# Optimization experiments

Hardware: AMD Instinct MI355X
Metric: run time of the kernel (lower is better)

The kernel has to match this reference:

```python
import jax, jax.numpy as jnp
import numpy as np

N_LEVELS = 16
N_FEATS = 2
LOG2_T = 19
BASE_RES = 16.0
FINEST_RES = 512.0
N_POINTS = 1048576

_PRIMES = jnp.array([1, 2654435761, 805459861], dtype=jnp.uint32)
_OFFSETS = jnp.array([[i, j, k] for i in (0, 1) for j in (0, 1) for k in (0, 1)], dtype=jnp.int32)  # [8,3]
_MASK = jnp.uint32(2 ** LOG2_T - 1)


def setup_inputs() -> dict:
    key = jax.random.key(0)
    k1, k2 = jax.random.split(key)
    x = jax.random.uniform(k1, (N_POINTS, 3), dtype=jnp.float32)
    # nn.init.uniform_(w, a=-1e-4, b=1e-4) per level; stacked [L, T, F]
    embeddings = jax.random.uniform(k2, (N_LEVELS, 2 ** LOG2_T, N_FEATS),
                                    dtype=jnp.float32, minval=-1e-4, maxval=1e-4)
    bounding_box = jnp.stack([jnp.zeros(3, jnp.float32), jnp.ones(3, jnp.float32)])  # [2,3]
    return {"x": x, "embeddings": embeddings, "bounding_box": bounding_box}


def _resolutions():
    b = np.exp((np.log(FINEST_RES) - np.log(BASE_RES)) / (N_LEVELS - 1))
    return jnp.asarray(np.floor(BASE_RES * b ** np.arange(N_LEVELS)), dtype=jnp.float32)  # [L]


def reference(x, embeddings, bounding_box):
    box_min, box_max = bounding_box[0], bounding_box[1]
    keep_mask = jnp.all((x >= box_min) & (x <= box_max), axis=-1)  # [N]
    xc = jnp.clip(x, box_min, box_max)  # clamped coords used for voxel indexing

    def level(emb, res):
        grid = (box_max - box_min) / res                              # [3]
        bl = jnp.floor((xc - box_min) / grid).astype(jnp.int32)       # [N,3] bottom-left voxel idx
        vmin = bl.astype(x.dtype) * grid + box_min                    # [N,3]
        w = (x - vmin) / grid                                         # [N,3] (original x, as in source)
        corners = bl[:, None, :] + _OFFSETS[None]                     # [N,8,3]
        h = corners.astype(jnp.uint32) * _PRIMES                      # wrap-around uint32 mul
        hashed = ((h[..., 0] ^ h[..., 1] ^ h[..., 2]) & _MASK).astype(jnp.int32)  # [N,8]
        v = emb[hashed]                                               # [N,8,F] gather
        wx, wy, wz = w[:, 0:1], w[:, 1:2], w[:, 2:3]
        c00 = v[:, 0] * (1 - wx) + v[:, 4] * wx
        c01 = v[:, 1] * (1 - wx) + v[:, 5] * wx
        c10 = v[:, 2] * (1 - wx) + v[:, 6] * wx
        c11 = v[:, 3] * (1 - wx) + v[:, 7] * wx
        c0 = c00 * (1 - wy) + c10 * wy
        c1 = c01 * (1 - wy) + c11 * wy
        return c0 * (1 - wz) + c1 * wz                                # [N,F]

    feats = jax.vmap(level)(embeddings, _resolutions())               # [L,N,F]
    out = jnp.transpose(feats, (1, 0, 2)).reshape(x.shape[0], N_LEVELS * N_FEATS)  # level-major concat
    return out, keep_mask
```

## Files before the change

kernel.cpp:

```cpp
#include <hip/hip_runtime.h>
#include <math.h>
#include <stdint.h>


#define NLEVELS 16
#define NFINE 10
#define HASH_MASK 0x7FFFFu
#define TABLE_ENTRIES 524288

typedef float f32x2 __attribute__((ext_vector_type(2)));
typedef float f32x4 __attribute__((ext_vector_type(4)));

struct ResTable { float r[NLEVELS]; };
struct PairMeta { int dim[6]; int off[6]; };

__device__ __forceinline__ float2 gather_one_level(
    const float* __restrict__ x, const float2* __restrict__ tbl,
    float bmin0, float bmin1, float bmin2,
    float bmax0, float bmax1, float bmax2,
    float res, int point)
{
    const float* xp = x + (size_t)point * 3;
    float x0 = __builtin_nontemporal_load(xp + 0);
    float x1 = __builtin_nontemporal_load(xp + 1);
    float x2 = __builtin_nontemporal_load(xp + 2);

    float xc0 = fminf(fmaxf(x0, bmin0), bmax0);
    float xc1 = fminf(fmaxf(x1, bmin1), bmax1);
    float xc2 = fminf(fmaxf(x2, bmin2), bmax2);

    float g0 = (bmax0 - bmin0) / res;
    float g1 = (bmax1 - bmin1) / res;
    float g2 = (bmax2 - bmin2) / res;

    float f0 = floorf((xc0 - bmin0) / g0);
    float f1 = floorf((xc1 - bmin1) / g1);
    float f2 = floorf((xc2 - bmin2) / g2);
    int b0 = (int)f0, b1 = (int)f1, b2 = (int)f2;

    float vmin0 = f0 * g0 + bmin0;
    float vmin1 = f1 * g1 + bmin1;
    float vmin2 = f2 * g2 + bmin2;
    float wx = (x0 - vmin0) / g0;
    float wy = (x1 - vmin1) / g1;
    float wz = (x2 - vmin2) / g2;

    uint32_t hx0 = (uint32_t)b0;
    uint32_t hx1 = (uint32_t)(b0 + 1);
    uint32_t hy0 = (uint32_t)b1 * 2654435761u;
    uint32_t hy1 = (uint32_t)(b1 + 1) * 2654435761u;
    uint32_t hz0 = (uint32_t)b2 * 805459861u;
    uint32_t hz1 = (uint32_t)(b2 + 1) * 805459861u;

    float2 v0 = tbl[(hx0 ^ hy0 ^ hz0) & HASH_MASK];
    float2 v1 = tbl[(hx0 ^ hy0 ^ hz1) & HASH_MASK];
    float2 v2 = tbl[(hx0 ^ hy1 ^ hz0) & HASH_MASK];
    float2 v3 = tbl[(hx0 ^ hy1 ^ hz1) & HASH_MASK];
    float2 v4 = tbl[(hx1 ^ hy0 ^ hz0) & HASH_MASK];
    float2 v5 = tbl[(hx1 ^ hy0 ^ hz1) & HASH_MASK];
    float2 v6 = tbl[(hx1 ^ hy1 ^ hz0) & HASH_MASK];
    float2 v7 = tbl[(hx1 ^ hy1 ^ hz1) & HASH_MASK];

    float omx = 1.0f - wx, omy = 1.0f - wy, omz = 1.0f - wz;

    float c00_0 = v0.x * omx + v4.x * wx;
    float c00_1 = v0.y * omx + v4.y * wx;
    float c01_0 = v1.x * omx + v5.x * wx;
    float c01_1 = v1.y * omx + v5.y * wx;
    float c10_0 = v2.x * omx + v6.x * wx;
    float c10_1 = v2.y * omx + v6.y * wx;
    float c11_0 = v3.x * omx + v7.x * wx;
    float c11_1 = v3.y * omx + v7.y * wx;

    float c0_0 = c00_0 * omy + c10_0 * wy;
    float c0_1 = c00_1 * omy + c10_1 * wy;
    float c1_0 = c01_0 * omy + c11_0 * wy;
    float c1_1 = c01_1 * omy + c11_1 * wy;

    float2 o;
    o.x = c0_0 * omz + c1_0 * wz;
    o.y = c0_1 * omz + c1_1 * wz;
    return o;
}

__device__ __forceinline__ void nt_store2(float2* p, float2 v) {
    f32x2 t = {v.x, v.y};
    __builtin_nontemporal_store(t, (f32x2*)p);
}

__global__ __launch_bounds__(256) void gather_hash8_kernel(
    const float* __restrict__ x,
    const float* __restrict__ emb,
    const float* __restrict__ bbox,
    float2* __restrict__ tmp,
    int n_points, int level_base, int tmp_lo, ResTable rt)
{
    int level = (blockIdx.x & 7) + level_base;
    int point = (blockIdx.x >> 3) * 256 + threadIdx.x;
    if (point >= n_points) return;

    float bmin0 = bbox[0], bmin1 = bbox[1], bmin2 = bbox[2];
    float bmax0 = bbox[3], bmax1 = bbox[4], bmax2 = bbox[5];

    const float2* tbl = (const float2*)emb + (size_t)level * TABLE_ENTRIES;
    float2 o = gather_one_level(x, tbl, bmin0, bmin1, bmin2,
                                bmax0, bmax1, bmax2, rt.r[level], point);
    nt_store2(&tmp[(size_t)(level - tmp_lo) * n_points + point], o);
}

__global__ __launch_bounds__(256) void gather_hash2_kernel(
    const float* __restrict__ x,
    const float* __restrict__ emb,
    const float* __restrict__ bbox,
    float2* __restrict__ tmp,
    int n_points, ResTable rt)
{
    int level = 6 + (blockIdx.x & 1);
    int point = (blockIdx.x >> 1) * 256 + threadIdx.x;
    if (point >= n_points) return;

    float bmin0 = bbox[0], bmin1 = bbox[1], bmin2 = bbox[2];
    float bmax0 = bbox[3], bmax1 = bbox[4], bmax2 = bbox[5];

    const float2* tbl = (const float2*)emb + (size_t)level * TABLE_ENTRIES;
    float2 o = gather_one_level(x, tbl, bmin0, bmin1, bmin2,
                                bmax0, bmax1, bmax2, rt.r[level], point);
    nt_store2(&tmp[(size_t)(level - 6) * n_points + point], o);
}

__global__ __launch_bounds__(256) void build_pair_kernel(
    const float* __restrict__ emb,
    float4* __restrict__ pair,
    PairMeta pm, int total)
{
    int id = blockIdx.x * 256 + threadIdx.x;
    if (id >= total) return;

    int l = 0;
#pragma unroll
    for (int t = 1; t < 6; ++t)
        if (id >= pm.off[t]) l = t;
    int local = id - pm.off[l];
    int D = pm.dim[l];
    int Dm = (D + 1) >> 1;

    int m = local % Dm;
    int t2 = local / Dm;
    int j = t2 % D;
    int i = t2 / D;
    int k0 = 2 * m, k1 = 2 * m + 1;

    uint32_t hij = (uint32_t)i ^ ((uint32_t)j * 2654435761u);
    uint32_t h0 = (hij ^ ((uint32_t)k0 * 805459861u)) & HASH_MASK;
    uint32_t h1 = (hij ^ ((uint32_t)k1 * 805459861u)) & HASH_MASK;
    const float2* tbl = (const float2*)emb + (size_t)l * TABLE_ENTRIES;
    float2 a = tbl[h0];
    float2 b = tbl[h1];
    pair[id] = make_float4(a.x, a.y, b.x, b.y);
}

__global__ __launch_bounds__(256) void fused_tail_kernel(
    const float* __restrict__ x,
    const float4* __restrict__ pair,
    const float2* __restrict__ tmp,
    const float* __restrict__ bbox,
    float* __restrict__ out,
    float* __restrict__ mask,
    int n_points, PairMeta pm, ResTable rt)
{
    __shared__ float lds[256 * 33];

    const int tid = threadIdx.x;
    const int p0 = blockIdx.x * 256;
    const int p = p0 + tid;

    if (p < n_points) {
        float bmin0 = bbox[0], bmin1 = bbox[1], bmin2 = bbox[2];
        float bmax0 = bbox[3], bmax1 = bbox[4], bmax2 = bbox[5];

        const float* xp = x + (size_t)p * 3;
        float x0 = __builtin_nontemporal_load(xp + 0);
        float x1 = __builtin_nontemporal_load(xp + 1);
        float x2 = __builtin_nontemporal_load(xp + 2);
        bool keep = (x0 >= bmin0) & (x0 <= bmax0) &
                    (x1 >= bmin1) & (x1 <= bmax1) &
                    (x2 >= bmin2) & (x2 <= bmax2);
        __builtin_nontemporal_store(keep ? 1.0f : 0.0f, &mask[p]);

        float xc0 = fminf(fmaxf(x0, bmin0), bmax0);
        float xc1 = fminf(fmaxf(x1, bmin1), bmax1);
        float xc2 = fminf(fmaxf(x2, bmin2), bmax2);

#pragma unroll
        for (int l = 0; l < 6; ++l) {
            float res = rt.r[l];
            float g0 = (bmax0 - bmin0) / res;
            float g1 = (bmax1 - bmin1) / res;
            float g2 = (bmax2 - bmin2) / res;

            float f0 = floorf((xc0 - bmin0) / g0);
            float f1 = floorf((xc1 - bmin1) / g1);
            float f2 = floorf((xc2 - bmin2) / g2);
            int b0 = (int)f0, b1 = (int)f1, b2 = (int)f2;

            float vmin0 = f0 * g0 + bmin0;
            float vmin1 = f1 * g1 + bmin1;
            float vmin2 = f2 * g2 + bmin2;
            float wx = (x0 - vmin0) / g0;
            float wy = (x1 - vmin1) / g1;
            float wz = (x2 - vmin2) / g2;

            int D = pm.dim[l];
            int Dm = (D + 1) >> 1;
            const float4* tb = pair + pm.off[l];

            int m0 = b2 >> 1;
            int r00 = (b0 * D + b1) * Dm;
            int r01 = r00 + Dm;
            int r10 = r00 + D * Dm;
            int r11 = r10 + Dm;

            float4 a00 = tb[r00 + m0];
            float4 a01 = tb[r01 + m0];
            float4 a10 = tb[r10 + m0];
            float4 a11 = tb[r11 + m0];

            float2 v0, v1, v2, v3, v4, v5, v6, v7;
            if (b2 & 1) {
                int m1 = m0 + 1;
                float4 e00 = tb[r00 + m1];
                float4 e01 = tb[r01 + m1];
                float4 e10 = tb[r10 + m1];
                float4 e11 = tb[r11 + m1];
                v0 = make_float2(a00.z, a00.w); v1 = make_float2(e00.x, e00.y);
                v2 = make_float2(a01.z, a01.w); v3 = make_float2(e01.x, e01.y);
                v4 = make_float2(a10.z, a10.w); v5 = make_float2(e10.x, e10.y);
                v6 = make_float2(a11.z, a11.w); v7 = make_float2(e11.x, e11.y);
            } else {
                v0 = make_float2(a00.x, a00.y); v1 = make_float2(a00.z, a00.w);
                v2 = make_float2(a01.x, a01.y); v3 = make_float2(a01.z, a01.w);
                v4 = make_float2(a10.x, a10.y); v5 = make_float2(a10.z, a10.w);
                v6 = make_float2(a11.x, a11.y); v7 = make_float2(a11.z, a11.w);
            }

            float omx = 1.0f - wx, omy = 1.0f - wy, omz = 1.0f - wz;

            float c00_0 = v0.x * omx + v4.x * wx;
            float c00_1 = v0.y * omx + v4.y * wx;
            float c01_0 = v1.x * omx + v5.x * wx;
            float c01_1 = v1.y * omx + v5.y * wx;
            float c10_0 = v2.x * omx + v6.x * wx;
            float c10_1 = v2.y * omx + v6.y * wx;
            float c11_0 = v3.x * omx + v7.x * wx;
            float c11_1 = v3.y * omx + v7.y * wx;

            float c0_0 = c00_0 * omy + c10_0 * wy;
            float c0_1 = c00_1 * omy + c10_1 * wy;
            float c1_0 = c01_0 * omy + c11_0 * wy;
            float c1_1 = c01_1 * omy + c11_1 * wy;

            lds[tid * 33 + 2 * l]     = c0_0 * omz + c1_0 * wz;
            lds[tid * 33 + 2 * l + 1] = c0_1 * omz + c1_1 * wz;
        }

#pragma unroll
        for (int l = 0; l < NFINE; ++l) {
            f32x2 v = __builtin_nontemporal_load(
                (const f32x2*)&tmp[(size_t)l * n_points + p]);
            lds[tid * 33 + 12 + 2 * l]     = v.x;
            lds[tid * 33 + 12 + 2 * l + 1] = v.y;
        }
    }

    __syncthreads();

    int nblk = n_points - p0;
    if (nblk > 256) nblk = 256;
    const int nfloat4 = nblk * 8;
    float* dst = out + (size_t)p0 * 32;
#pragma unroll
    for (int j = 0; j < 8; ++j) {
        int v = j * 256 + tid;
        if (v < nfloat4) {
            int q = v >> 3;
            int k = (v & 7) << 2;
            const float* s = &lds[q * 33 + k];
            f32x4 val = {s[0], s[1], s[2], s[3]};
            __builtin_nontemporal_store(val, (f32x4*)(dst + v * 4));
        }
    }
}

__global__ __launch_bounds__(256) void assemble_lds_kernel(
    const float* __restrict__ x,
    const float2* __restrict__ tmp,
    const float* __restrict__ bbox,
    float* __restrict__ out,
    float* __restrict__ mask,
    int n_points)
{
    __shared__ float lds[256 * 33];

    const int tid = threadIdx.x;
    const int p0 = blockIdx.x * 256;
    const int p = p0 + tid;

    if (p < n_points) {
#pragma unroll
        for (int l = 0; l < NLEVELS; ++l) {
            float2 v = tmp[(size_t)l * n_points + p];
            lds[tid * 33 + 2 * l]     = v.x;
            lds[tid * 33 + 2 * l + 1] = v.y;
        }
        float bmin0 = bbox[0], bmin1 = bbox[1], bmin2 = bbox[2];
        float bmax0 = bbox[3], bmax1 = bbox[4], bmax2 = bbox[5];
        const float* xp = x + (size_t)p * 3;
        float x0 = xp[0], x1 = xp[1], x2 = xp[2];
        bool keep = (x0 >= bmin0) & (x0 <= bmax0) &
                    (x1 >= bmin1) & (x1 <= bmax1) &
                    (x2 >= bmin2) & (x2 <= bmax2);
        mask[p] = keep ? 1.0f : 0.0f;
    }

    __syncthreads();

    int nblk = n_points - p0;
    if (nblk > 256) nblk = 256;
    const int nfloat4 = nblk * 8;
    float4* dst = (float4*)(out + (size_t)p0 * 32);
#pragma unroll
    for (int j = 0; j < 8; ++j) {
        int v = j * 256 + tid;
        if (v < nfloat4) {
            int q = v >> 3;
            int k = (v & 7) << 2;
            const float* s = &lds[q * 33 + k];
            dst[v] = make_float4(s[0], s[1], s[2], s[3]);
        }
    }
}

__global__ __launch_bounds__(256) void hash_embed_direct_kernel(
    const float* __restrict__ x,
    const float* __restrict__ emb,
    const float* __restrict__ bbox,
    float* __restrict__ out,
    float* __restrict__ mask,
    int n_points, ResTable rt)
{
    int tid = blockIdx.x * 256 + threadIdx.x;
    int point = tid >> 4;
    int level = tid & 15;
    if (point >= n_points) return;

    float bmin0 = bbox[0], bmin1 = bbox[1], bmin2 = bbox[2];
    float bmax0 = bbox[3], bmax1 = bbox[4], bmax2 = bbox[5];

    if (level == 0) {
        const float* xp = x + (size_t)point * 3;
        float x0 = xp[0], x1 = xp[1], x2 = xp[2];
        bool keep = (x0 >= bmin0) & (x0 <= bmax0) &
                    (x1 >= bmin1) & (x1 <= bmax1) &
                    (x2 >= bmin2) & (x2 <= bmax2);
        mask[point] = keep ? 1.0f : 0.0f;
    }

    const float2* tbl = (const float2*)emb + (size_t)level * TABLE_ENTRIES;
    float2 o = gather_one_level(x, tbl, bmin0, bmin1, bmin2,
                                bmax0, bmax1, bmax2, rt.r[level], point);
    *(float2*)(out + (size_t)point * 32 + level * 2) = o;
}

extern "C" void kernel_launch(void* const* d_in, const int* in_sizes, int n_in,
                              void* d_out, int out_size, void* d_ws, size_t ws_size,
                              hipStream_t stream) {
    const float* x    = (const float*)d_in[0];
    const float* emb  = (const float*)d_in[1];
    const float* bbox = (const float*)d_in[2];
    int n_points = in_sizes[0] / 3;

    float* out  = (float*)d_out;
    float* mask = out + (size_t)n_points * 32;

    ResTable rt;
    double b = exp((log(512.0) - log(16.0)) / 15.0);
    for (int l = 0; l < NLEVELS; ++l)
        rt.r[l] = (float)floor(16.0 * pow(b, (double)l));

    PairMeta pm;
    int total_cells = 0;
    for (int l = 0; l < 6; ++l) {
        int D = (int)rt.r[l] + 2;
        pm.dim[l] = D;
        pm.off[l] = total_cells;
        total_cells += D * D * ((D + 1) >> 1);
    }

    size_t tmp10_bytes = (size_t)n_points * NFINE * sizeof(float2);
    size_t tmp16_bytes = (size_t)n_points * NLEVELS * sizeof(float2);
    size_t pair_bytes  = (size_t)total_cells * sizeof(float4);

    int chunks = (n_points + 255) / 256;

    if (ws_size >= tmp10_bytes + pair_bytes) {
        float2* tmp  = (float2*)d_ws;
        float4* pair = (float4*)((char*)d_ws + tmp10_bytes);

        int pre_blocks = (total_cells + 255) / 256;
        hipLaunchKernelGGL(build_pair_kernel, dim3(pre_blocks), dim3(256),
                           0, stream, emb, pair, pm, total_cells);

        hipLaunchKernelGGL(gather_hash8_kernel, dim3(chunks * 8), dim3(256),
                           0, stream, x, emb, bbox, tmp, n_points, 8, 6, rt);
        hipLaunchKernelGGL(gather_hash2_kernel, dim3(chunks * 2), dim3(256),
                           0, stream, x, emb, bbox, tmp, n_points, rt);
        hipLaunchKernelGGL(fused_tail_kernel, dim3(chunks), dim3(256),
                           0, stream, x, pair, tmp, bbox, out, mask,
                           n_points, pm, rt);
    } else if (ws_size >= tmp16_bytes) {
        float2* tmp = (float2*)d_ws;
        dim3 grid(chunks * 8);
        hipLaunchKernelGGL(gather_hash8_kernel, grid, dim3(256), 0, stream,
                           x, emb, bbox, tmp, n_points, 0, 0, rt);
        hipLaunchKernelGGL(gather_hash8_kernel, grid, dim3(256), 0, stream,
                           x, emb, bbox, tmp, n_points, 8, 0, rt);
        hipLaunchKernelGGL(assemble_lds_kernel, dim3(chunks), dim3(256), 0,
                           stream, x, tmp, bbox, out, mask, n_points);
    } else {
        long long total = (long long)n_points * NLEVELS;
        int blocks = (int)((total + 255) / 256);
        hipLaunchKernelGGL(hash_embed_direct_kernel, dim3(blocks), dim3(256), 0,
                           stream, x, emb, bbox, out, mask, n_points, rt);
    }
}
```

Baseline: 594.5 us.

## Use overlapping pair table for coarse levels, merge gather kernels, prefetch fine features

```diff
diff --git a/kernel.cpp b/kernel.cpp
--- a/kernel.cpp
+++ b/kernel.cpp
@@ -88,15 +88,18 @@
     __builtin_nontemporal_store(t, (f32x2*)p);
 }
 
-__global__ __launch_bounds__(256) void gather_hash8_kernel(
+__global__ __launch_bounds__(256) void gather_hash_kernel(
     const float* __restrict__ x,
     const float* __restrict__ emb,
     const float* __restrict__ bbox,
     float2* __restrict__ tmp,
-    int n_points, int level_base, int tmp_lo, ResTable rt)
-{
-    int level = (blockIdx.x & 7) + level_base;
-    int point = (blockIdx.x >> 3) * 256 + threadIdx.x;
+    int n_points, int chunks8, ResTable rt)
+{
+    int b = blockIdx.x;
+    int level, pchunk;
+    if (b < chunks8) { level = 8 + (b & 7); pchunk = b >> 3; }
+    else             { int c = b - chunks8; level = 6 + (c & 1); pchunk = c >> 1; }
+    int point = pchunk * 256 + threadIdx.x;
     if (point >= n_points) return;
 
     float bmin0 = bbox[0], bmin1 = bbox[1], bmin2 = bbox[2];
@@ -105,18 +108,18 @@
     const float2* tbl = (const float2*)emb + (size_t)level * TABLE_ENTRIES;
     float2 o = gather_one_level(x, tbl, bmin0, bmin1, bmin2,
                                 bmax0, bmax1, bmax2, rt.r[level], point);
-    nt_store2(&tmp[(size_t)(level - tmp_lo) * n_points + point], o);
-}
-
-__global__ __launch_bounds__(256) void gather_hash2_kernel(
+    nt_store2(&tmp[(size_t)(level - 6) * n_points + point], o);
+}
+
+__global__ __launch_bounds__(256) void gather_level_kernel(
     const float* __restrict__ x,
     const float* __restrict__ emb,
     const float* __restrict__ bbox,
     float2* __restrict__ tmp,
-    int n_points, ResTable rt)
-{
-    int level = 6 + (blockIdx.x & 1);
-    int point = (blockIdx.x >> 1) * 256 + threadIdx.x;
+    int n_points, int level_base, ResTable rt)
+{
+    int level = (blockIdx.x & 7) + level_base;
+    int point = (blockIdx.x >> 3) * 256 + threadIdx.x;
     if (point >= n_points) return;
 
     float bmin0 = bbox[0], bmin1 = bbox[1], bmin2 = bbox[2];
@@ -125,7 +128,7 @@
     const float2* tbl = (const float2*)emb + (size_t)level * TABLE_ENTRIES;
     float2 o = gather_one_level(x, tbl, bmin0, bmin1, bmin2,
                                 bmax0, bmax1, bmax2, rt.r[level], point);
-    nt_store2(&tmp[(size_t)(level - 6) * n_points + point], o);
+    nt_store2(&tmp[(size_t)level * n_points + point], o);
 }
 
 __global__ __launch_bounds__(256) void build_pair_kernel(
@@ -142,13 +145,20 @@
         if (id >= pm.off[t]) l = t;
     int local = id - pm.off[l];
     int D = pm.dim[l];
-    int Dm = (D + 1) >> 1;
-
-    int m = local % Dm;
-    int t2 = local / Dm;
-    int j = t2 % D;
-    int i = t2 / D;
-    int k0 = 2 * m, k1 = 2 * m + 1;
+
+    int i, j, k0, k1;
+    if (l < 4) {
+        int k = local % D;
+        int t2 = local / D;
+        j = t2 % D; i = t2 / D;
+        k0 = k; k1 = k + 1;
+    } else {
+        int Dm = (D + 1) >> 1;
+        int m = local % Dm;
+        int t2 = local / Dm;
+        j = t2 % D; i = t2 / D;
+        k0 = 2 * m; k1 = 2 * m + 1;
+    }
 
     uint32_t hij = (uint32_t)i ^ ((uint32_t)j * 2654435761u);
     uint32_t h0 = (hij ^ ((uint32_t)k0 * 805459861u)) & HASH_MASK;
@@ -182,6 +192,13 @@
         float x0 = __builtin_nontemporal_load(xp + 0);
         float x1 = __builtin_nontemporal_load(xp + 1);
         float x2 = __builtin_nontemporal_load(xp + 2);
+
+        f32x2 tv[NFINE];
+#pragma unroll
+        for (int l = 0; l < NFINE; ++l)
+            tv[l] = __builtin_nontemporal_load(
+                (const f32x2*)&tmp[(size_t)l * n_points + p]);
+
         bool keep = (x0 >= bmin0) & (x0 <= bmax0) &
                     (x1 >= bmin1) & (x1 <= bmax1) &
                     (x2 >= bmin2) & (x2 <= bmax2);
@@ -211,36 +228,49 @@
             float wz = (x2 - vmin2) / g2;
 
             int D = pm.dim[l];
-            int Dm = (D + 1) >> 1;
             const float4* tb = pair + pm.off[l];
 
-            int m0 = b2 >> 1;
-            int r00 = (b0 * D + b1) * Dm;
-            int r01 = r00 + Dm;
-            int r10 = r00 + D * Dm;
-            int r11 = r10 + Dm;
-
-            float4 a00 = tb[r00 + m0];
-            float4 a01 = tb[r01 + m0];
-            float4 a10 = tb[r10 + m0];
-            float4 a11 = tb[r11 + m0];
-
             float2 v0, v1, v2, v3, v4, v5, v6, v7;
-            if (b2 & 1) {
-                int m1 = m0 + 1;
-                float4 e00 = tb[r00 + m1];
-                float4 e01 = tb[r01 + m1];
-                float4 e10 = tb[r10 + m1];
-                float4 e11 = tb[r11 + m1];
-                v0 = make_float2(a00.z, a00.w); v1 = make_float2(e00.x, e00.y);
-                v2 = make_float2(a01.z, a01.w); v3 = make_float2(e01.x, e01.y);
-                v4 = make_float2(a10.z, a10.w); v5 = make_float2(e10.x, e10.y);
-                v6 = make_float2(a11.z, a11.w); v7 = make_float2(e11.x, e11.y);
-            } else {
+            if (l < 4) {
+                int c = (b0 * D + b1) * D + b2;
+                int dj = D, di = D * D;
+                float4 a00 = tb[c];
+                float4 a01 = tb[c + dj];
+                float4 a10 = tb[c + di];
+                float4 a11 = tb[c + di + dj];
                 v0 = make_float2(a00.x, a00.y); v1 = make_float2(a00.z, a00.w);
                 v2 = make_float2(a01.x, a01.y); v3 = make_float2(a01.z, a01.w);
                 v4 = make_float2(a10.x, a10.y); v5 = make_float2(a10.z, a10.w);
                 v6 = make_float2(a11.x, a11.y); v7 = make_float2(a11.z, a11.w);
+            } else {
+                int Dm = (D + 1) >> 1;
+                int m0 = b2 >> 1;
+                int r00 = (b0 * D + b1) * Dm;
+                int r01 = r00 + Dm;
+                int r10 = r00 + D * Dm;
+                int r11 = r10 + Dm;
+
+                float4 a00 = tb[r00 + m0];
+                float4 a01 = tb[r01 + m0];
+                float4 a10 = tb[r10 + m0];
+                float4 a11 = tb[r11 + m0];
+
+                if (b2 & 1) {
+                    int m1 = m0 + 1;
+                    float4 e00 = tb[r00 + m1];
+                    float4 e01 = tb[r01 + m1];
+                    float4 e10 = tb[r10 + m1];
+                    float4 e11 = tb[r11 + m1];
+                    v0 = make_float2(a00.z, a00.w); v1 = make_float2(e00.x, e00.y);
+                    v2 = make_float2(a01.z, a01.w); v3 = make_float2(e01.x, e01.y);
+                    v4 = make_float2(a10.z, a10.w); v5 = make_float2(e10.x, e10.y);
+                    v6 = make_float2(a11.z, a11.w); v7 = make_float2(e11.x, e11.y);
+                } else {
+                    v0 = make_float2(a00.x, a00.y); v1 = make_float2(a00.z, a00.w);
+                    v2 = make_float2(a01.x, a01.y); v3 = make_float2(a01.z, a01.w);
+                    v4 = make_float2(a10.x, a10.y); v5 = make_float2(a10.z, a10.w);
+                    v6 = make_float2(a11.x, a11.y); v7 = make_float2(a11.z, a11.w);
+                }
             }
 
             float omx = 1.0f - wx, omy = 1.0f - wy, omz = 1.0f - wz;
@@ -265,10 +295,8 @@
 
 #pragma unroll
         for (int l = 0; l < NFINE; ++l) {
-            f32x2 v = __builtin_nontemporal_load(
-                (const f32x2*)&tmp[(size_t)l * n_points + p]);
-            lds[tid * 33 + 12 + 2 * l]     = v.x;
-            lds[tid * 33 + 12 + 2 * l + 1] = v.y;
+            lds[tid * 33 + 12 + 2 * l]     = tv[l].x;
+            lds[tid * 33 + 12 + 2 * l + 1] = tv[l].y;
         }
     }
 
@@ -393,7 +421,7 @@
         int D = (int)rt.r[l] + 2;
         pm.dim[l] = D;
         pm.off[l] = total_cells;
-        total_cells += D * D * ((D + 1) >> 1);
+        total_cells += (l < 4) ? D * D * D : D * D * ((D + 1) >> 1);
     }
 
     size_t tmp10_bytes = (size_t)n_points * NFINE * sizeof(float2);
@@ -410,20 +438,21 @@
         hipLaunchKernelGGL(build_pair_kernel, dim3(pre_blocks), dim3(256),
                            0, stream, emb, pair, pm, total_cells);
 
-        hipLaunchKernelGGL(gather_hash8_kernel, dim3(chunks * 8), dim3(256),
-                           0, stream, x, emb, bbox, tmp, n_points, 8, 6, rt);
-        hipLaunchKernelGGL(gather_hash2_kernel, dim3(chunks * 2), dim3(256),
-                           0, stream, x, emb, bbox, tmp, n_points, rt);
+        int chunks8 = chunks * 8;
+        hipLaunchKernelGGL(gather_hash_kernel,
+                           dim3(chunks8 + chunks * 2), dim3(256),
+                           0, stream, x, emb, bbox, tmp, n_points, chunks8, rt);
+
         hipLaunchKernelGGL(fused_tail_kernel, dim3(chunks), dim3(256),
                            0, stream, x, pair, tmp, bbox, out, mask,
                            n_points, pm, rt);
     } else if (ws_size >= tmp16_bytes) {
         float2* tmp = (float2*)d_ws;
         dim3 grid(chunks * 8);
-        hipLaunchKernelGGL(gather_hash8_kernel, grid, dim3(256), 0, stream,
-                           x, emb, bbox, tmp, n_points, 0, 0, rt);
-        hipLaunchKernelGGL(gather_hash8_kernel, grid, dim3(256), 0, stream,
-                           x, emb, bbox, tmp, n_points, 8, 0, rt);
+        hipLaunchKernelGGL(gather_level_kernel, grid, dim3(256), 0, stream,
+                           x, emb, bbox, tmp, n_points, 0, rt);
+        hipLaunchKernelGGL(gather_level_kernel, grid, dim3(256), 0, stream,
+                           x, emb, bbox, tmp, n_points, 8, rt);
         hipLaunchKernelGGL(assemble_lds_kernel, dim3(chunks), dim3(256), 0,
                            stream, x, tmp, bbox, out, mask, n_points);
     } else {
```

Result: faster. 552.9 us (-7.0%).
